# Kernel optimization log

Hardware: AMD Instinct MI355X
Metric: run time of the kernel (lower is better)

## Reference

```python
import jax, jax.numpy as jnp
import numpy as np

B, S, T, F, H, DEPTH = 8, 96, 96, 64, 64, 2


def setup_inputs() -> dict:
    key = jax.random.key(0)
    ks = jax.random.split(key, 10)
    scale = np.float32(1.0 / np.sqrt(H))
    rn = lambda k, sh: jax.random.normal(k, sh, dtype=jnp.float32)
    return {
        "src": rn(ks[0], (B, S, F)),
        "trg": rn(ks[1], (B, T, F)),
        "Wi_x": rn(ks[2], (DEPTH, F, H)) * scale,
        "Wh_x": rn(ks[3], (DEPTH, 2 * H, H)) * scale,
        "b_x": jnp.zeros((DEPTH, H), jnp.float32),
        "Wi_y": rn(ks[4], (DEPTH, F, H)) * scale,
        "Wh_y": rn(ks[5], (DEPTH, 2 * H, H)) * scale,
        "b_y": jnp.zeros((DEPTH, H), jnp.float32),
        "src_lens": jax.random.randint(ks[6], (B,), 1, S + 1),
        "trg_lens": jax.random.randint(ks[7], (B,), 1, T + 1),
    }


def _grid_layer(px, py, Whx, bx, Why, by):
    # px, py: (B, S, T, H) precomputed input projections (x @ Wi).
    # Wavefront recurrence: h_prev = [h_x(i-1,j), h_y(i,j-1)] (zeros at borders),
    # h_x(i,j) = tanh(px + h_prev @ Whx + bx), h_y(i,j) = tanh(py + h_prev @ Why + by).
    Bn, Sn, Tn, Hn = px.shape

    def row_step(hx_above_row, row_in):
        pxr, pyr = row_in  # (T, B, H) each

        def col_step(hy_left, col_in):
            pxc, pyc, hx_above = col_in  # (B, H) each
            h_prev = jnp.concatenate([hx_above, hy_left], axis=-1)  # (B, 2H)
            hx = jnp.tanh(pxc + h_prev @ Whx + bx)
            hy = jnp.tanh(pyc + h_prev @ Why + by)
            return hy, (hx, hy)

        _, (hx_row, hy_row) = jax.lax.scan(
            col_step, jnp.zeros((Bn, Hn), px.dtype), (pxr, pyr, hx_above_row))
        return hx_row, (hx_row, hy_row)

    px_t = jnp.transpose(px, (1, 2, 0, 3))  # (S, T, B, H)
    py_t = jnp.transpose(py, (1, 2, 0, 3))
    _, (hx, hy) = jax.lax.scan(
        row_step, jnp.zeros((Tn, Bn, Hn), px.dtype), (px_t, py_t))
    return jnp.transpose(hx, (2, 0, 1, 3)), jnp.transpose(hy, (2, 0, 1, 3))


def _forward(src, trg, Wi_x, Wh_x, b_x, Wi_y, Wh_y, b_y, src_lens, trg_lens):
    hx = hy = None
    hxs, hys = [], []
    for d in range(DEPTH):
        if d == 0:
            # depth 0: x input depends only on i, y input only on j
            px = jnp.broadcast_to((src @ Wi_x[0])[:, :, None, :], (B, S, T, H))
            py = jnp.broadcast_to((trg @ Wi_y[0])[:, None, :, :], (B, S, T, H))
        else:
            # depth d>0: inputs are previous depth's x/y outputs at the same (i,j)
            px = jnp.einsum('bsth,hk->bstk', hx, Wi_x[d])
            py = jnp.einsum('bsth,hk->bstk', hy, Wi_y[d])
        hx, hy = _grid_layer(px, py, Wh_x[d], b_x[d], Wh_y[d], b_y[d])
        hxs.append(hx)
        hys.append(hy)
    # zero out points outside each sample's (src_len x trg_len) valid grid
    mask = ((jnp.arange(S)[None, :, None] < src_lens[:, None, None])
            & (jnp.arange(T)[None, None, :] < trg_lens[:, None, None]))
    mask = mask[:, :, :, None].astype(src.dtype)  # (B, S, T, 1)
    out = jnp.stack([jnp.stack(hxs), jnp.stack(hys)])  # (2, DEPTH, B, S, T, H)
    return out * mask


_forward_jit = jax.jit(_forward)


def reference(src, trg, Wi_x, Wh_x, b_x, Wi_y, Wh_y, b_y, src_lens, trg_lens):
    return _forward_jit(src, trg, Wi_x, Wh_x, b_x, Wi_y, Wh_y, b_y,
                        src_lens, trg_lens)
```

## Files before the change

kernel.cpp:

```cpp
#include <hip/hip_runtime.h>

typedef unsigned short u16;
typedef unsigned int   u32;
typedef _Float16 f16x8 __attribute__((ext_vector_type(8)));
typedef float  f32x2  __attribute__((ext_vector_type(2)));
typedef float  f32x4  __attribute__((ext_vector_type(4)));
typedef int    i32x4  __attribute__((ext_vector_type(4)));
typedef u32    u32x2  __attribute__((ext_vector_type(2)));

#define Bn 8
#define Sn 96
#define Tn 96
#define Hn 64
#define H2n 128
#define STRB 152
#define ARRB 16384
#define STATEB 131072
#define PXROW 152
#define PXG   (Sn*PXROW)
#define PXBASE STATEB
#define LDSB  (STATEB + 2*PXG)
#define ODS 24320
#define TSTP 2432

__device__ __forceinline__ int imax(int a, int b){ return a > b ? a : b; }
__device__ __forceinline__ int imin(int a, int b){ return a < b ? a : b; }

__device__ __forceinline__ u32 pack2f16(float a, float b){
  _Float16 ha = (_Float16)a, hb = (_Float16)b;
  return (u32)__builtin_bit_cast(u16, ha) | ((u32)__builtin_bit_cast(u16, hb) << 16);
}
__device__ __forceinline__ float f16tof(u32 v){
  return (float)__builtin_bit_cast(_Float16, (u16)v);
}
__device__ __forceinline__ float fast_tanh(float x){
  float e = exp2f(x * 2.88539008f);
  return __builtin_fmaf(-2.f, __builtin_amdgcn_rcpf(e + 1.f), 1.f);
}
__device__ __forceinline__ void barrier_lds_only(){
  asm volatile("s_waitcnt vmcnt(63) expcnt(7) lgkmcnt(0)\n\ts_barrier" ::: "memory");
}
__device__ __forceinline__ f16x8 ld_state(const char* p){
  u32x2 a = *(const u32x2*)(p);
  u32x2 b = *(const u32x2*)(p + 8);
  i32x4 v; v[0] = (int)a[0]; v[1] = (int)a[1]; v[2] = (int)b[0]; v[3] = (int)b[1];
  return __builtin_bit_cast(f16x8, v);
}

__global__ __launch_bounds__(64) void proj0_kernel(
  const float* __restrict__ src, const float* __restrict__ trg,
  const float* __restrict__ Wix, const float* __restrict__ Wiy,
  const float* __restrict__ bx, const float* __restrict__ by,
  float* __restrict__ ws)
{
  const int row = blockIdx.x, g = blockIdx.y, b = blockIdx.z;
  const int n = threadIdx.x;
  const float* x = (g == 0) ? (src + (b*Sn + row)*Hn) : (trg + (b*Tn + row)*Hn);
  const float* W = (g == 0) ? Wix : Wiy;
  float a = (g == 0) ? bx[n] : by[n];
  #pragma unroll 8
  for (int f = 0; f < Hn; ++f) a = fmaf(x[f], W[f*Hn + n], a);
  ws[((size_t)(b*2 + g)*Sn + row)*Hn + n] = a;
}

__global__ __launch_bounds__(1024, 1) void grid_rnn_fused(
  const float* __restrict__ Whx, const float* __restrict__ Why,
  const float* __restrict__ Wix, const float* __restrict__ Wiy,
  const float* __restrict__ bx,  const float* __restrict__ by,
  const int* __restrict__ src_lens, const int* __restrict__ trg_lens,
  float* __restrict__ out, const float* __restrict__ ws)
{
  extern __shared__ u16 smem[];
  char* const smemc = (char*)smem;
  const int b    = blockIdx.x;
  const int tid  = threadIdx.x;
  const int lane = tid & 63;
  const int wid  = __builtin_amdgcn_readfirstlane(tid >> 6);
  const int q    = lane >> 4;
  const int c    = lane & 15;
  const int dep  = wid & 1;
  const int nt   = (wid >> 1) & 3;
  const int g    = wid >> 3;
  const int sl = __builtin_amdgcn_readfirstlane(src_lens[b]);
  const int tl = __builtin_amdgcn_readfirstlane(trg_lens[b]);
  const int NB = sl + tl;

  for (int idx = tid; idx < STATEB/16; idx += 1024) ((i32x4*)smem)[idx] = (i32x4)(0);

  {
    const int gp = tid >> 9;
    const int t5 = tid & 511;
    const float* wsg = ws + (size_t)(b*2 + gp)*Sn*Hn;
    #pragma unroll
    for (int it = 0; it < 6; ++it){
      int w = t5 + it*512;
      int row = w >> 5, pr = w & 31;
      f32x2 v = *(const f32x2*)(wsg + row*64 + pr*2);
      *(u32*)(smemc + PXBASE + gp*PXG + row*PXROW + pr*4) = pack2f16(v[0], v[1]);
    }
  }

  const float* Wh = (g == 0 ? Whx : Why) + dep*H2n*Hn;
  const int nb = nt*16 + c;
  i32x4 whf[4];
  #pragma unroll
  for (int kk = 0; kk < 4; ++kk)
    #pragma unroll
    for (int p = 0; p < 4; ++p){
      float w0 = Wh[(kk*32 + q*8 + 2*p    )*Hn + nb];
      float w1 = Wh[(kk*32 + q*8 + 2*p + 1)*Hn + nb];
      whf[kk][p] = (int)pack2f16(w0, w1);
    }
  const float* Wi = (g == 0 ? Wix : Wiy) + Hn*Hn;
  i32x4 wif[2];
  #pragma unroll
  for (int kk = 0; kk < 2; ++kk)
    #pragma unroll
    for (int p = 0; p < 4; ++p){
      float w0 = Wi[(kk*32 + q*8 + 2*p    )*Hn + nb];
      float w1 = Wi[(kk*32 + q*8 + 2*p + 1)*Hn + nb];
      wif[kk][p] = (int)pack2f16(w0, w1);
    }
  f32x4 bias4;
  {
    const float* bb = (g == 0 ? bx : by) + dep*Hn;
    #pragma unroll
    for (int r4 = 0; r4 < 4; ++r4) bias4[r4] = bb[nt*16 + q*4 + r4];
  }
  char* const outb = (char*)(out + (size_t)((g*2 + dep)*Bn + b)*(size_t)(Sn*Tn)*Hn);

  const int plX  = q*16 - c*STRB;
  const int plY  = q*16 + c*STRB;
  const int plP  = g ? plY : plX;
  const int plW  = (g ? c*STRB : -c*STRB) + nt*32 + q*8;
  const int plPx = (g ? -c*PXROW : c*PXROW) + nt*32 + q*8;
  const int plO  = c*ODS + nt*64 + q*16;

  const int depB   = dep*4*ARRB;
  const int basePg = g ? 2*ARRB : 0;
  const int baseWg = depB + (g ? 2*ARRB : 0);

  __syncthreads();

  for (int r = 0; r < NB; ++r){
    const int myd  = r - dep;
    const bool wact = (myd >= 0) && (myd <= NB - 2);
    const int cpB = (r & 1) ? ARRB : 0;
    const int ppB = ARRB - cpB;
    const int i0 = imax(0, myd - (tl - 1));
    const int i1 = imin(sl - 1, myd);
    const int nc = i1 - i0 + 1;
    const int mtiles = (nc + 15) >> 4;
    const int rJ0 = myd - i0, rJm = myd - i1;
    const int aX  = depB + ppB + rJ0*STRB;
    const int loX = depB + ppB + rJm*STRB;
    const int aY  = depB + 2*ARRB + ppB + i0*STRB;
    const int hiY = depB + 2*ARRB + ppB + i1*STRB + 48;
    const int aP  = basePg + ppB + (g ? i0 : rJ0)*STRB;
    const int loP = basePg + ppB + (g ? i0 : rJm)*STRB;
    const int hiP = basePg + ppB + (g ? i1 : rJ0)*STRB + 48;
    const int aW  = baseWg + cpB + (g ? i0 : rJ0)*STRB;
    const int aPx = PXBASE + g*PXG + (g ? rJ0 : i0)*PXROW;
    const int loPx= PXBASE + g*PXG + (g ? rJm : i0)*PXROW;
    const int hiPx= PXBASE + g*PXG + (g ? rJ0 : i1)*PXROW + 120;
    const int sO  = myd*256 + i0*ODS;

    #pragma unroll
    for (int u = 0; u < 6; ++u){
      if (!(wact && u < mtiles)) continue;
      const int du = u*TSTP;

      int vX = aX - du + plX; vX = imax(vX, loX);
      int vY = aY + du + plY; vY = imin(vY, hiY);

      f32x4 acc;
      if (dep == 0){
        int vp = aPx + (g ? -du : du) + plPx;
        vp = imin(imax(vp, loPx), hiPx);
        u32x2 pv = *(const u32x2*)(smemc + vp);
        acc[0] = f16tof(pv[0] & 0xffffu); acc[1] = f16tof(pv[0] >> 16);
        acc[2] = f16tof(pv[1] & 0xffffu); acc[3] = f16tof(pv[1] >> 16);
      } else {
        acc = bias4;
      }
      #pragma unroll
      for (int kk = 0; kk < 2; ++kk){
        f16x8 sv = ld_state(smemc + vX + kk*64);
        acc = __builtin_amdgcn_mfma_f32_16x16x32_f16(
                __builtin_bit_cast(f16x8, whf[kk]), sv, acc, 0, 0, 0);
      }
      #pragma unroll
      for (int kk = 0; kk < 2; ++kk){
        f16x8 sv = ld_state(smemc + vY + kk*64);
        acc = __builtin_amdgcn_mfma_f32_16x16x32_f16(
                __builtin_bit_cast(f16x8, whf[kk+2]), sv, acc, 0, 0, 0);
      }
      if (dep == 1){
        int vP = aP + (g ? du : -du) + plP;
        vP = imin(imax(vP, loP), hiP);
        #pragma unroll
        for (int kk = 0; kk < 2; ++kk){
          f16x8 pv = ld_state(smemc + vP + kk*64);
          acc = __builtin_amdgcn_mfma_f32_16x16x32_f16(
                  __builtin_bit_cast(f16x8, wif[kk]), pv, acc, 0, 0, 0);
        }
      }
      float h0 = fast_tanh(acc[0]), h1 = fast_tanh(acc[1]);
      float h2 = fast_tanh(acc[2]), h3 = fast_tanh(acc[3]);
      if (c < nc - u*16){
        const int vW = aW + (g ? du : -du) + plW;
        u32x2 hp; hp[0] = pack2f16(h0, h1); hp[1] = pack2f16(h2, h3);
        *(u32x2*)(smemc + vW) = hp;
        f32x4 ov = {h0, h1, h2, h3};
        *(f32x4*)(outb + (u32)(sO + u*(16*ODS) + plO)) = ov;
      }
    }
    barrier_lds_only();
  }
}

extern "C" void kernel_launch(void* const* d_in, const int* in_sizes, int n_in,
                              void* d_out, int out_size, void* d_ws, size_t ws_size,
                              hipStream_t stream) {
  (void)in_sizes; (void)n_in; (void)ws_size;
  (void)hipFuncSetAttribute((const void*)grid_rnn_fused,
                            hipFuncAttributeMaxDynamicSharedMemorySize, LDSB);
  (void)hipMemsetAsync(d_out, 0, (size_t)out_size, stream);
  proj0_kernel<<<dim3(Sn, 2, Bn), 64, 0, stream>>>(
      (const float*)d_in[0], (const float*)d_in[1],
      (const float*)d_in[2], (const float*)d_in[5],
      (const float*)d_in[4], (const float*)d_in[7],
      (float*)d_ws);
  grid_rnn_fused<<<dim3(Bn), dim3(1024), LDSB, stream>>>(
      (const float*)d_in[3], (const float*)d_in[6],
      (const float*)d_in[2], (const float*)d_in[5],
      (const float*)d_in[4], (const float*)d_in[7],
      (const int*)d_in[8], (const int*)d_in[9],
      (float*)d_out, (const float*)d_ws);
}
```

Measured before the change: 506.4 us.

## Split wave work by column tiles so each wave computes two output feature tiles

```diff
diff --git a/kernel.cpp b/kernel.cpp
--- a/kernel.cpp
+++ b/kernel.cpp
@@ -79,7 +79,8 @@
   const int q    = lane >> 4;
   const int c    = lane & 15;
   const int dep  = wid & 1;
-  const int nt   = (wid >> 1) & 3;
+  const int nh   = (wid >> 1) & 1;
+  const int ch   = (wid >> 2) & 1;
   const int g    = wid >> 3;
   const int sl = __builtin_amdgcn_readfirstlane(src_lens[b]);
   const int tl = __builtin_amdgcn_readfirstlane(trg_lens[b]);
@@ -101,40 +102,49 @@
   }
 
   const float* Wh = (g == 0 ? Whx : Why) + dep*H2n*Hn;
-  const int nb = nt*16 + c;
-  i32x4 whf[4];
+  i32x4 whf[4][2];
   #pragma unroll
   for (int kk = 0; kk < 4; ++kk)
     #pragma unroll
-    for (int p = 0; p < 4; ++p){
-      float w0 = Wh[(kk*32 + q*8 + 2*p    )*Hn + nb];
-      float w1 = Wh[(kk*32 + q*8 + 2*p + 1)*Hn + nb];
-      whf[kk][p] = (int)pack2f16(w0, w1);
+    for (int fc = 0; fc < 2; ++fc){
+      const int nb = nh*32 + fc*16 + c;
+      #pragma unroll
+      for (int p = 0; p < 4; ++p){
+        float w0 = Wh[(kk*32 + q*8 + 2*p    )*Hn + nb];
+        float w1 = Wh[(kk*32 + q*8 + 2*p + 1)*Hn + nb];
+        whf[kk][fc][p] = (int)pack2f16(w0, w1);
+      }
     }
   const float* Wi = (g == 0 ? Wix : Wiy) + Hn*Hn;
-  i32x4 wif[2];
+  i32x4 wif[2][2];
   #pragma unroll
   for (int kk = 0; kk < 2; ++kk)
     #pragma unroll
-    for (int p = 0; p < 4; ++p){
-      float w0 = Wi[(kk*32 + q*8 + 2*p    )*Hn + nb];
-      float w1 = Wi[(kk*32 + q*8 + 2*p + 1)*Hn + nb];
-      wif[kk][p] = (int)pack2f16(w0, w1);
-    }
-  f32x4 bias4;
+    for (int fc = 0; fc < 2; ++fc){
+      const int nb = nh*32 + fc*16 + c;
+      #pragma unroll
+      for (int p = 0; p < 4; ++p){
+        float w0 = Wi[(kk*32 + q*8 + 2*p    )*Hn + nb];
+        float w1 = Wi[(kk*32 + q*8 + 2*p + 1)*Hn + nb];
+        wif[kk][fc][p] = (int)pack2f16(w0, w1);
+      }
+    }
+  f32x4 bias4[2];
   {
     const float* bb = (g == 0 ? bx : by) + dep*Hn;
     #pragma unroll
-    for (int r4 = 0; r4 < 4; ++r4) bias4[r4] = bb[nt*16 + q*4 + r4];
+    for (int fc = 0; fc < 2; ++fc)
+      #pragma unroll
+      for (int r4 = 0; r4 < 4; ++r4) bias4[fc][r4] = bb[nh*32 + fc*16 + q*4 + r4];
   }
   char* const outb = (char*)(out + (size_t)((g*2 + dep)*Bn + b)*(size_t)(Sn*Tn)*Hn);
 
   const int plX  = q*16 - c*STRB;
   const int plY  = q*16 + c*STRB;
   const int plP  = g ? plY : plX;
-  const int plW  = (g ? c*STRB : -c*STRB) + nt*32 + q*8;
-  const int plPx = (g ? -c*PXROW : c*PXROW) + nt*32 + q*8;
-  const int plO  = c*ODS + nt*64 + q*16;
+  const int plW  = (g ? c*STRB : -c*STRB) + nh*64 + q*8;
+  const int plPx = (g ? -c*PXROW : c*PXROW) + nh*64 + q*8;
+  const int plO  = c*ODS + nh*128 + q*16;
 
   const int depB   = dep*4*ARRB;
   const int basePg = g ? 2*ARRB : 0;
@@ -162,38 +172,50 @@
     const int aW  = baseWg + cpB + (g ? i0 : rJ0)*STRB;
     const int aPx = PXBASE + g*PXG + (g ? rJ0 : i0)*PXROW;
     const int loPx= PXBASE + g*PXG + (g ? rJm : i0)*PXROW;
-    const int hiPx= PXBASE + g*PXG + (g ? rJ0 : i1)*PXROW + 120;
+    const int hiPx= PXBASE + g*PXG + (g ? rJ0 : i1)*PXROW + 88;
     const int sO  = myd*256 + i0*ODS;
 
     #pragma unroll
-    for (int u = 0; u < 6; ++u){
+    for (int t = 0; t < 3; ++t){
+      const int u = ch + 2*t;
       if (!(wact && u < mtiles)) continue;
       const int du = u*TSTP;
 
       int vX = aX - du + plX; vX = imax(vX, loX);
       int vY = aY + du + plY; vY = imin(vY, hiY);
 
-      f32x4 acc;
+      f16x8 bvx[2], bvy[2];
+      #pragma unroll
+      for (int kk = 0; kk < 2; ++kk) bvx[kk] = ld_state(smemc + vX + kk*64);
+      #pragma unroll
+      for (int kk = 0; kk < 2; ++kk) bvy[kk] = ld_state(smemc + vY + kk*64);
+
+      f32x4 a0, a1;
       if (dep == 0){
         int vp = aPx + (g ? -du : du) + plPx;
         vp = imin(imax(vp, loPx), hiPx);
-        u32x2 pv = *(const u32x2*)(smemc + vp);
-        acc[0] = f16tof(pv[0] & 0xffffu); acc[1] = f16tof(pv[0] >> 16);
-        acc[2] = f16tof(pv[1] & 0xffffu); acc[3] = f16tof(pv[1] >> 16);
+        u32x2 p0 = *(const u32x2*)(smemc + vp);
+        u32x2 p1 = *(const u32x2*)(smemc + vp + 32);
+        a0[0] = f16tof(p0[0] & 0xffffu); a0[1] = f16tof(p0[0] >> 16);
+        a0[2] = f16tof(p0[1] & 0xffffu); a0[3] = f16tof(p0[1] >> 16);
+        a1[0] = f16tof(p1[0] & 0xffffu); a1[1] = f16tof(p1[0] >> 16);
+        a1[2] = f16tof(p1[1] & 0xffffu); a1[3] = f16tof(p1[1] >> 16);
       } else {
-        acc = bias4;
+        a0 = bias4[0]; a1 = bias4[1];
       }
       #pragma unroll
       for (int kk = 0; kk < 2; ++kk){
-        f16x8 sv = ld_state(smemc + vX + kk*64);
-        acc = __builtin_amdgcn_mfma_f32_16x16x32_f16(
-                __builtin_bit_cast(f16x8, whf[kk]), sv, acc, 0, 0, 0);
+        a0 = __builtin_amdgcn_mfma_f32_16x16x32_f16(
+               __builtin_bit_cast(f16x8, whf[kk][0]), bvx[kk], a0, 0, 0, 0);
+        a1 = __builtin_amdgcn_mfma_f32_16x16x32_f16(
+               __builtin_bit_cast(f16x8, whf[kk][1]), bvx[kk], a1, 0, 0, 0);
       }
       #pragma unroll
       for (int kk = 0; kk < 2; ++kk){
-        f16x8 sv = ld_state(smemc + vY + kk*64);
-        acc = __builtin_amdgcn_mfma_f32_16x16x32_f16(
-                __builtin_bit_cast(f16x8, whf[kk+2]), sv, acc, 0, 0, 0);
+        a0 = __builtin_amdgcn_mfma_f32_16x16x32_f16(
+               __builtin_bit_cast(f16x8, whf[kk+2][0]), bvy[kk], a0, 0, 0, 0);
+        a1 = __builtin_amdgcn_mfma_f32_16x16x32_f16(
+               __builtin_bit_cast(f16x8, whf[kk+2][1]), bvy[kk], a1, 0, 0, 0);
       }
       if (dep == 1){
         int vP = aP + (g ? du : -du) + plP;
@@ -201,18 +223,27 @@
         #pragma unroll
         for (int kk = 0; kk < 2; ++kk){
           f16x8 pv = ld_state(smemc + vP + kk*64);
-          acc = __builtin_amdgcn_mfma_f32_16x16x32_f16(
-                  __builtin_bit_cast(f16x8, wif[kk]), pv, acc, 0, 0, 0);
+          a0 = __builtin_amdgcn_mfma_f32_16x16x32_f16(
+                 __builtin_bit_cast(f16x8, wif[kk][0]), pv, a0, 0, 0, 0);
+          a1 = __builtin_amdgcn_mfma_f32_16x16x32_f16(
+                 __builtin_bit_cast(f16x8, wif[kk][1]), pv, a1, 0, 0, 0);
         }
       }
-      float h0 = fast_tanh(acc[0]), h1 = fast_tanh(acc[1]);
-      float h2 = fast_tanh(acc[2]), h3 = fast_tanh(acc[3]);
+      float h0 = fast_tanh(a0[0]), h1 = fast_tanh(a0[1]);
+      float h2 = fast_tanh(a0[2]), h3 = fast_tanh(a0[3]);
+      float h4 = fast_tanh(a1[0]), h5 = fast_tanh(a1[1]);
+      float h6 = fast_tanh(a1[2]), h7 = fast_tanh(a1[3]);
       if (c < nc - u*16){
         const int vW = aW + (g ? du : -du) + plW;
-        u32x2 hp; hp[0] = pack2f16(h0, h1); hp[1] = pack2f16(h2, h3);
-        *(u32x2*)(smemc + vW) = hp;
-        f32x4 ov = {h0, h1, h2, h3};
-        *(f32x4*)(outb + (u32)(sO + u*(16*ODS) + plO)) = ov;
+        u32x2 hp0; hp0[0] = pack2f16(h0, h1); hp0[1] = pack2f16(h2, h3);
+        u32x2 hp1; hp1[0] = pack2f16(h4, h5); hp1[1] = pack2f16(h6, h7);
+        *(u32x2*)(smemc + vW) = hp0;
+        *(u32x2*)(smemc + vW + 32) = hp1;
+        char* oa = outb + (u32)(sO + u*(16*ODS) + plO);
+        f32x4 ov0 = {h0, h1, h2, h3};
+        f32x4 ov1 = {h4, h5, h6, h7};
+        *(f32x4*)(oa) = ov0;
+        *(f32x4*)(oa + 64) = ov1;
       }
     }
     barrier_lds_only();
```

New measurement: 458.7 us. -9.4%, faster.
